# Optimization experiments

Measured on AMD Instinct MI355X. Metric: run time of the kernel, lower is better.

Reference implementation:

```python
import jax, jax.numpy as jnp
import numpy as np

N = 8192
BOX = 50.0
CUTOFF = 5.0
MAX_E = 64 * N  # padded edge capacity (~34 avg neighbors expected)


def setup_inputs() -> dict:
    key = jax.random.key(0)
    pos = jax.random.uniform(key, (N, 3), dtype=jnp.float32) * BOX
    return {"pos": pos}


def _pairwise_dist(pos):
    # Euclidean cdist via the gram-matrix identity; avoids the [N,N,3] intermediate.
    sq = jnp.sum(pos * pos, axis=-1)                      # [N]
    d2 = sq[:, None] + sq[None, :] - 2.0 * (pos @ pos.T)  # [N,N]
    return jnp.sqrt(jnp.maximum(d2, 0.0))


def reference(pos):
    n = pos.shape[0]
    dist = _pairwise_dist(pos)
    # mask self-edges by pushing the diagonal above the cutoff (as in the torch code)
    dist = dist + (CUTOFF + 1.0) * jnp.eye(n, dtype=dist.dtype)
    mask = dist < CUTOFF
    # data-dependent nonzero -> fixed-size padded output for jit compatibility;
    # padded entries are filled with -1.
    rows, cols = jnp.nonzero(mask, size=MAX_E, fill_value=-1)
    return jnp.stack([rows, cols], axis=0)  # [2, MAX_E], int32
```

## Files before the change

kernel.cpp:

```cpp
#include <hip/hip_runtime.h>
#include <stdint.h>

#define N 8192
#define MAX_E (64 * N)
#define NCHUNK (N / 64)
#define NCOL1 9
#define NCOLS (NCOL1 * NCOL1)
#define CAP 256
#define SCALE (9.0f / 50.0f)
#define POISON 0xAAAAAAAAu
#define M_WAVES 4
#define E_BLOCKS 512
#define E_ROWS 16

__device__ __forceinline__ float sq_exact(float x, float y, float z) {
    return __fadd_rn(__fadd_rn(__fmul_rn(x, x), __fmul_rn(y, y)), __fmul_rn(z, z));
}

__device__ __forceinline__ bool edge_pred(float xi, float yi, float zi, float sqi,
                                          const float4& pj) {
    float dot = __fmaf_rn(zi, pj.z, __fmaf_rn(yi, pj.y, __fmul_rn(xi, pj.x)));
    float d2  = __fmaf_rn(-2.0f, dot, __fadd_rn(sqi, pj.w));
    return d2 < 0x1.8ffffep+4f;
}

__device__ __forceinline__ int cell_of(float v) {
    int c = (int)(__fmul_rn(v, SCALE));
    return c > 8 ? 8 : c;
}

__global__ __launch_bounds__(256) void bin_kernel(const float* __restrict__ posf,
                                                  unsigned* __restrict__ gcount,
                                                  float4* __restrict__ colpts,
                                                  int* __restrict__ colidx) {
    const int i = blockIdx.x * 256 + threadIdx.x;
    float x = posf[3 * i], y = posf[3 * i + 1], z = posf[3 * i + 2];
    int col = cell_of(x) * NCOL1 + cell_of(y);
    unsigned p = atomicAdd(&gcount[col], 1u) - POISON;
    if (p < CAP) {
        colpts[col * CAP + p] = make_float4(x, y, z, sq_exact(x, y, z));
        colidx[col * CAP + p] = i;
    }
}

__global__ __launch_bounds__(256) void mask_kernel(const float* __restrict__ posf,
                                                   const unsigned* __restrict__ gcount,
                                                   const float4* __restrict__ colpts,
                                                   const int* __restrict__ colidx,
                                                   uint64_t* __restrict__ masks,
                                                   int* __restrict__ counts) {
    __shared__ uint32_t lmask[M_WAVES][256];
    const int tid  = threadIdx.x;
    const int wave = tid >> 6;
    const int lane = tid & 63;
    const int row  = blockIdx.x * M_WAVES + wave;

#pragma unroll
    for (int k = lane; k < 256; k += 64) lmask[wave][k] = 0;

    const float xi = posf[3 * row], yi = posf[3 * row + 1], zi = posf[3 * row + 2];
    const float sqi = sq_exact(xi, yi, zi);
    const int cx = cell_of(xi), cy = cell_of(yi);
    __syncthreads();

    for (int dx = -1; dx <= 1; dx++) {
        const int nx = cx + dx;
        if ((unsigned)nx > 8u) continue;
        for (int dy = -1; dy <= 1; dy++) {
            const int ny = cy + dy;
            if ((unsigned)ny > 8u) continue;
            const int col = nx * NCOL1 + ny;
            int cnt = (int)(gcount[col] - POISON);
            if (cnt > CAP) cnt = CAP;
            for (int base = 0; base < cnt; base += 64) {
                const int k = base + lane;
                if (k < cnt) {
                    float4 pj = colpts[col * CAP + k];
                    int j = colidx[col * CAP + k];
                    if (j != row && edge_pred(xi, yi, zi, sqi, pj))
                        atomicOr(&lmask[wave][j >> 5], 1u << (j & 31));
                }
            }
        }
    }
    __syncthreads();

    uint4 u = ((const uint4*)lmask[wave])[lane];
    uint64_t k0 = (uint64_t)u.x | ((uint64_t)u.y << 32);
    uint64_t k1 = (uint64_t)u.z | ((uint64_t)u.w << 32);
    ulonglong2 v; v.x = k0; v.y = k1;
    ((ulonglong2*)(masks + (size_t)row * NCHUNK))[lane] = v;
    int t = __popcll(k0) + __popcll(k1);
#pragma unroll
    for (int o = 32; o > 0; o >>= 1) t += __shfl_down(t, o);
    if (lane == 0) counts[row] = t;
}

__global__ __launch_bounds__(256) void emit_kernel(const uint64_t* __restrict__ masks,
                                                   const int* __restrict__ counts,
                                                   int* __restrict__ out) {
    const int tid  = threadIdx.x;
    const int wave = tid >> 6;
    const int lane = tid & 63;
    const int row0 = blockIdx.x * E_ROWS;

    __shared__ int part[256];
    __shared__ int excl32[32];

    const int4* c4 = (const int4*)counts;
    int s = 0;
#pragma unroll
    for (int k = 0; k < 8; k++) {
        int4 v = c4[tid * 8 + k];
        s += v.x + v.y + v.z + v.w;
    }
    part[tid] = s;
    const int ch = row0 >> 5;
    if (tid < 32) excl32[tid] = counts[(ch << 5) + tid];
    __syncthreads();
    for (int off = 1; off < 256; off <<= 1) {
        int v = (tid >= off) ? part[tid - off] : 0;
        __syncthreads();
        part[tid] += v;
        __syncthreads();
    }
    if (tid == 0) {
        int run = 0;
#pragma unroll
        for (int k = 0; k < 32; k++) { int c = excl32[k]; excl32[k] = run; run += c; }
    }
    __syncthreads();
    const int base = (ch > 0) ? part[ch - 1] : 0;
    const int E    = part[255];
    const int sub  = row0 & 31;

    for (int idx = E + blockIdx.x * 256 + tid; idx < MAX_E; idx += E_BLOCKS * 256) {
        out[idx] = -1; out[MAX_E + idx] = -1;
    }

#pragma unroll
    for (int r = 0; r < 4; r++) {
        const int lr  = wave * 4 + r;
        const int row = row0 + lr;
        ulonglong2 v = ((const ulonglong2*)(masks + (size_t)row * NCHUNK))[lane];
        int s0 = __popcll(v.x), s1 = __popcll(v.y);
        int x = s0 + s1;
#pragma unroll
        for (int o = 1; o < 64; o <<= 1) {
            int t = __shfl_up(x, o);
            if (lane >= o) x += t;
        }
        int slot = base + excl32[sub + lr] + (x - (s0 + s1));

        const int col0 = lane * 128;
        uint64_t m = v.x;
        while (m) {
            int b = __ffsll((unsigned long long)m) - 1;
            m &= m - 1;
            if (slot < MAX_E) { out[slot] = row; out[MAX_E + slot] = col0 + b; }
            slot++;
        }
        m = v.y;
        while (m) {
            int b = __ffsll((unsigned long long)m) - 1;
            m &= m - 1;
            if (slot < MAX_E) { out[slot] = row; out[MAX_E + slot] = col0 + 64 + b; }
            slot++;
        }
    }
}

extern "C" void kernel_launch(void* const* d_in, const int* in_sizes, int n_in,
                              void* d_out, int out_size, void* d_ws, size_t ws_size,
                              hipStream_t stream) {
    const float* posf = (const float*)d_in[0];
    int* out = (int*)d_out;
    char* ws = (char*)d_ws;
    int*      counts = (int*)ws;
    unsigned* gcount = (unsigned*)(ws + (64 << 10));
    int*      colidx = (int*)(ws + (128 << 10));
    float4*   colpts = (float4*)(ws + (256 << 10));
    uint64_t* masks  = (uint64_t*)(ws + (1 << 20));

    bin_kernel<<<N / 256, 256, 0, stream>>>(posf, gcount, colpts, colidx);
    mask_kernel<<<N / M_WAVES, 256, 0, stream>>>(posf, gcount, colpts, colidx,
                                                 masks, counts);
    emit_kernel<<<E_BLOCKS, 256, 0, stream>>>(masks, counts, out);
}
```

Before: 86.82 us.

## Use wave-shuffle block scan and 32 rows per emit block

```diff
diff --git a/kernel.cpp b/kernel.cpp
--- a/kernel.cpp
+++ b/kernel.cpp
@@ -10,8 +10,8 @@
 #define SCALE (9.0f / 50.0f)
 #define POISON 0xAAAAAAAAu
 #define M_WAVES 4
-#define E_BLOCKS 512
-#define E_ROWS 16
+#define E_BLOCKS 256
+#define E_ROWS 32
 
 __device__ __forceinline__ float sq_exact(float x, float y, float z) {
     return __fadd_rn(__fadd_rn(__fmul_rn(x, x), __fmul_rn(y, y)), __fmul_rn(z, z));
@@ -105,7 +105,8 @@
     const int row0 = blockIdx.x * E_ROWS;
 
     __shared__ int part[256];
-    __shared__ int excl32[32];
+    __shared__ int wtot[4];
+    __shared__ int excl32[E_ROWS];
 
     const int4* c4 = (const int4*)counts;
     int s = 0;
@@ -114,43 +115,45 @@
         int4 v = c4[tid * 8 + k];
         s += v.x + v.y + v.z + v.w;
     }
-    part[tid] = s;
-    const int ch = row0 >> 5;
-    if (tid < 32) excl32[tid] = counts[(ch << 5) + tid];
+    int x = s;
+#pragma unroll
+    for (int o = 1; o < 64; o <<= 1) {
+        int t = __shfl_up(x, o);
+        if (lane >= o) x += t;
+    }
+    if (lane == 63) wtot[wave] = x;
+    if (tid < E_ROWS) excl32[tid] = counts[row0 + tid];
     __syncthreads();
-    for (int off = 1; off < 256; off <<= 1) {
-        int v = (tid >= off) ? part[tid - off] : 0;
-        __syncthreads();
-        part[tid] += v;
-        __syncthreads();
-    }
+    int add = 0;
+#pragma unroll
+    for (int w = 0; w < 4; w++) add += (w < wave) ? wtot[w] : 0;
+    part[tid] = x + add;
     if (tid == 0) {
         int run = 0;
 #pragma unroll
-        for (int k = 0; k < 32; k++) { int c = excl32[k]; excl32[k] = run; run += c; }
+        for (int k = 0; k < E_ROWS; k++) { int c = excl32[k]; excl32[k] = run; run += c; }
     }
     __syncthreads();
-    const int base = (ch > 0) ? part[ch - 1] : 0;
+    const int base = (blockIdx.x > 0) ? part[blockIdx.x - 1] : 0;
     const int E    = part[255];
-    const int sub  = row0 & 31;
 
     for (int idx = E + blockIdx.x * 256 + tid; idx < MAX_E; idx += E_BLOCKS * 256) {
         out[idx] = -1; out[MAX_E + idx] = -1;
     }
 
 #pragma unroll
-    for (int r = 0; r < 4; r++) {
-        const int lr  = wave * 4 + r;
+    for (int r = 0; r < 8; r++) {
+        const int lr  = wave * 8 + r;
         const int row = row0 + lr;
         ulonglong2 v = ((const ulonglong2*)(masks + (size_t)row * NCHUNK))[lane];
         int s0 = __popcll(v.x), s1 = __popcll(v.y);
-        int x = s0 + s1;
+        int p = s0 + s1;
 #pragma unroll
         for (int o = 1; o < 64; o <<= 1) {
-            int t = __shfl_up(x, o);
-            if (lane >= o) x += t;
+            int t = __shfl_up(p, o);
+            if (lane >= o) p += t;
         }
-        int slot = base + excl32[sub + lr] + (x - (s0 + s1));
+        int slot = base + excl32[lr] + (p - (s0 + s1));
 
         const int col0 = lane * 128;
         uint64_t m = v.x;
```

Measured after the change: 89.65 us. +3.3%, slower.
